# Kernel optimization log

Measured on AMD Instinct MI355X. Metric: run time of the kernel, lower is better.

The kernel has to match this reference:

```python
import jax, jax.numpy as jnp
import numpy as np

N_NODES = 50000
N_EDGES = 800000
IN_F = 128
HID = 16
HEADS = 8
OUT_F = 128


def setup_inputs() -> dict:
    key = jax.random.key(0)
    ks = jax.random.split(key, 16)
    h = jax.random.normal(ks[0], (N_NODES, IN_F), dtype=jnp.float32)
    src1 = jax.random.randint(ks[1], (N_EDGES,), 0, N_NODES, dtype=jnp.int32)
    dst1 = jax.random.randint(ks[2], (N_EDGES,), 0, N_NODES, dtype=jnp.int32)
    src2 = jax.random.randint(ks[3], (N_EDGES,), 0, N_NODES, dtype=jnp.int32)
    dst2 = jax.random.randint(ks[4], (N_EDGES,), 0, N_NODES, dtype=jnp.int32)
    norm1 = jax.random.uniform(ks[5], (N_NODES, 1), dtype=jnp.float32)
    norm2 = jax.random.uniform(ks[6], (N_NODES, 1), dtype=jnp.float32)
    D = HEADS * HID  # 128
    W_lin = jax.random.normal(ks[7], (IN_F, D), dtype=jnp.float32) * (1.0 / np.sqrt(IN_F))
    b_lin = jax.random.normal(ks[8], (D,), dtype=jnp.float32) * 0.01
    al = jax.random.normal(ks[9], (HEADS, HID, 1), dtype=jnp.float32) * 0.1
    ar = jax.random.normal(ks[10], (HEADS, HID, 1), dtype=jnp.float32) * 0.1
    W_fc = jax.random.normal(ks[11], (D, OUT_F), dtype=jnp.float32) * (1.0 / np.sqrt(D))
    b_fc = jax.random.normal(ks[12], (OUT_F,), dtype=jnp.float32) * 0.01
    return {"h": h, "src1": src1, "dst1": dst1, "src2": src2, "dst2": dst2,
            "norm1": norm1, "norm2": norm2, "W_lin": W_lin, "b_lin": b_lin,
            "al": al, "ar": ar, "W_fc": W_fc, "b_fc": b_fc}


def _propagate(feat, norm, src, dst, n_nodes):
    # msg = h[src] * norm[src]; accum[v] = sum_{e: dst=v} msg_e; out = accum * norm
    msg = feat[src] * norm[src]                      # [E, D]
    agg = jax.ops.segment_sum(msg, dst, num_segments=n_nodes)
    return agg * norm                                # [N, D]


def _leaky_relu(x):
    return jnp.where(x > 0, x, 0.2 * x)


def reference(h, src1, dst1, src2, dst2, norm1, norm2, W_lin, b_lin, al, ar, W_fc, b_fc):
    N = h.shape[0]
    hf = h @ W_lin + b_lin                           # [N, 8*HID] (dropout p given but eval-mode -> identity)
    h1 = _propagate(hf, norm1, src1, dst1, N)
    h2 = _propagate(hf, norm2, src2, dst2, N)
    # Faithful to torch: row-major reshape [N, 8*HID] -> (8, N, HID)
    h1r = h1.reshape(HEADS, N, HID)
    h2r = h2.reshape(HEADS, N, HID)
    hr = hf.reshape(HEADS, N, HID)
    ai = jnp.einsum('hnd,hdo->hno', hr, al)          # [8, N, 1]
    aj1 = jnp.einsum('hnd,hdo->hno', h1r, ar)
    aj2 = jnp.einsum('hnd,hdo->hno', h2r, ar)
    a1 = jnp.clip(jnp.exp(_leaky_relu(ai + aj1)), -10.0, 10.0)
    a2 = jnp.clip(jnp.exp(_leaky_relu(ai + aj2)), -10.0, 10.0)
    denom = a1 + a2
    out = (a1 / denom) * h1r + (a2 / denom) * h2r    # [8, N, HID]
    out = out.reshape(N, HEADS * HID)
    return out @ W_fc + b_fc
```

## Files before the change

### kernel.cpp

```cpp
#include <hip/hip_runtime.h>

#define NN 50000
#define NE 800000
#define NB 196
#define NBLK 512
#define CHUNK 1563
#define MAXB 6144

typedef __bf16 bf16x8 __attribute__((ext_vector_type(8)));
typedef float  f32x4  __attribute__((ext_vector_type(4)));

__device__ __forceinline__ unsigned short f2bf(float x) {
    unsigned u = __float_as_uint(x);
    return (unsigned short)((u + 0x7FFFu + ((u >> 16) & 1u)) >> 16);
}
__device__ __forceinline__ float bflo(unsigned u) { return __uint_as_float(u << 16); }
__device__ __forceinline__ float bfhi(unsigned u) { return __uint_as_float(u & 0xFFFF0000u); }

__global__ __launch_bounds__(256) void mfma_gemm_kernel(
    const float* __restrict__ X, const float* __restrict__ W,
    const float* __restrict__ bias, float* __restrict__ Y,
    unsigned short* __restrict__ Ybf, int nrows)
{
    __shared__ unsigned short Wt[128 * 136];
    __shared__ unsigned short Xh[64 * 136];
    __shared__ unsigned short Xl[64 * 136];
    const int t = threadIdx.x;
    const int lane = t & 63;
    const int wv = t >> 6;
    const int row0 = blockIdx.x * 64;
    const int m16 = lane & 15;
    const int quad = lane >> 4;

    for (int i = t; i < 128 * 128; i += 256) {
        int k = i >> 7, n = i & 127;
        Wt[n * 136 + k] = f2bf(W[i]);
    }
    {
        const float4* X4 = (const float4*)X;
        #pragma unroll
        for (int i = 0; i < 8; i++) {
            int idx = t + i * 256;
            int rr = idx >> 5, kk = (idx & 31) * 4;
            int row = row0 + rr;
            float4 v = make_float4(0.f, 0.f, 0.f, 0.f);
            if (row < nrows) v = X4[(long)row * 32 + (idx & 31)];
            ushort4 h, l;
            h.x = f2bf(v.x); l.x = f2bf(v.x - bflo(h.x));
            h.y = f2bf(v.y); l.y = f2bf(v.y - bflo(h.y));
            h.z = f2bf(v.z); l.z = f2bf(v.z - bflo(h.z));
            h.w = f2bf(v.w); l.w = f2bf(v.w - bflo(h.w));
            *(ushort4*)&Xh[rr * 136 + kk] = h;
            *(ushort4*)&Xl[rr * 136 + kk] = l;
        }
    }
    __syncthreads();

    f32x4 acc[8];
    #pragma unroll
    for (int nt = 0; nt < 8; nt++) acc[nt] = (f32x4){0.f, 0.f, 0.f, 0.f};

    const int arow = wv * 16 + m16;
    #pragma unroll
    for (int kc = 0; kc < 4; kc++) {
        const int ko = kc * 32 + quad * 8;
        bf16x8 ah = *(const bf16x8*)&Xh[arow * 136 + ko];
        bf16x8 al = *(const bf16x8*)&Xl[arow * 136 + ko];
        #pragma unroll
        for (int nt = 0; nt < 8; nt++) {
            bf16x8 b = *(const bf16x8*)&Wt[(nt * 16 + m16) * 136 + ko];
            acc[nt] = __builtin_amdgcn_mfma_f32_16x16x32_bf16(ah, b, acc[nt], 0, 0, 0);
            acc[nt] = __builtin_amdgcn_mfma_f32_16x16x32_bf16(al, b, acc[nt], 0, 0, 0);
        }
    }

    #pragma unroll
    for (int nt = 0; nt < 8; nt++) {
        const int col = nt * 16 + m16;
        const float bc = bias[col];
        #pragma unroll
        for (int r = 0; r < 4; r++) {
            int row = row0 + wv * 16 + quad * 4 + r;
            if (row < nrows) {
                float val = acc[nt][r] + bc;
                if (Y)   Y[(long)row * 128 + col] = val;
                if (Ybf) Ybf[(long)row * 128 + col] = f2bf(val);
            }
        }
    }
}

__global__ __launch_bounds__(256) void histA_kernel(
    const int* __restrict__ dst1, const int* __restrict__ dst2, int* __restrict__ histG)
{
    __shared__ int h[2 * NB];
    const int t = threadIdx.x, blk = blockIdx.x;
    for (int i = t; i < 2 * NB; i += 256) h[i] = 0;
    __syncthreads();
    const int base = blk * CHUNK;
    const int lim = min(CHUNK, NE - base);
    for (int i = t; i < lim; i += 256) {
        atomicAdd(&h[dst1[base + i] >> 8], 1);
        atomicAdd(&h[NB + (dst2[base + i] >> 8)], 1);
    }
    __syncthreads();
    for (int i = t; i < 2 * NB; i += 256)
        histG[(size_t)i * NBLK + blk] = h[i];
}

__global__ __launch_bounds__(512) void scanB1_kernel(int* __restrict__ histG, int* __restrict__ btot)
{
    __shared__ int s[NBLK];
    const int t = threadIdx.x, row = blockIdx.x;
    int v = histG[(size_t)row * NBLK + t];
    s[t] = v;
    __syncthreads();
    for (int off = 1; off < NBLK; off <<= 1) {
        int x = (t >= off) ? s[t - off] : 0;
        __syncthreads();
        s[t] += x;
        __syncthreads();
    }
    histG[(size_t)row * NBLK + t] = s[t] - v;
    if (t == NBLK - 1) btot[row] = s[t];
}

__global__ __launch_bounds__(256) void scanB2_kernel(const int* __restrict__ btot, int* __restrict__ bbase)
{
    __shared__ int sc[256];
    const int t = threadIdx.x;
    for (int g = 0; g < 2; g++) {
        int v = (t < NB) ? btot[g * NB + t] : 0;
        sc[t] = v;
        __syncthreads();
        for (int off = 1; off < 256; off <<= 1) {
            int x = (t >= off) ? sc[t - off] : 0;
            __syncthreads();
            sc[t] += x;
            __syncthreads();
        }
        if (t < NB) bbase[g * NB + t] = sc[t] - v;
        __syncthreads();
    }
}

__global__ __launch_bounds__(256) void scatterC_kernel(
    const int* __restrict__ src1, const int* __restrict__ dst1,
    const int* __restrict__ src2, const int* __restrict__ dst2,
    const int* __restrict__ histG, const int* __restrict__ bbase,
    unsigned int* __restrict__ bin1, unsigned int* __restrict__ bin2)
{
    __shared__ int pos[2 * NB];
    const int t = threadIdx.x, blk = blockIdx.x;
    for (int i = t; i < 2 * NB; i += 256)
        pos[i] = bbase[i] + histG[(size_t)i * NBLK + blk];
    __syncthreads();
    const int base = blk * CHUNK;
    const int lim = min(CHUNK, NE - base);
    for (int i = t; i < lim; i += 256) {
        int d = dst1[base + i], s = src1[base + i];
        int slot = atomicAdd(&pos[d >> 8], 1);
        bin1[slot] = ((unsigned)(d & 255) << 16) | (unsigned)s;
        d = dst2[base + i]; s = src2[base + i];
        slot = atomicAdd(&pos[NB + (d >> 8)], 1);
        bin2[slot] = ((unsigned)(d & 255) << 16) | (unsigned)s;
    }
}

__global__ __launch_bounds__(256) void bucket_sort_kernel(
    const unsigned int* __restrict__ bin1, const unsigned int* __restrict__ bin2,
    const int* __restrict__ bbase, const int* __restrict__ btot,
    unsigned short* __restrict__ csr1, int* __restrict__ start1, int* __restrict__ deg1,
    unsigned short* __restrict__ csr2, int* __restrict__ start2, int* __restrict__ deg2)
{
    __shared__ int lcnt[256];
    __shared__ int sc[256];
    __shared__ int oat[256];
    __shared__ unsigned short outb[MAXB];
    const int t = threadIdx.x;
    const int g = (blockIdx.x >= NB) ? 1 : 0;
    const int b = blockIdx.x - g * NB;
    const unsigned int* bin = g ? bin2 : bin1;
    unsigned short* csr = g ? csr2 : csr1;
    int* start = g ? start2 : start1;
    int* deg   = g ? deg2 : deg1;

    const int base = bbase[g * NB + b];
    const int tot = min(btot[g * NB + b], MAXB);

    lcnt[t] = 0;
    __syncthreads();
    for (int i = t; i < tot; i += 256) atomicAdd(&lcnt[bin[base + i] >> 16], 1);
    __syncthreads();
    sc[t] = lcnt[t];
    __syncthreads();
    for (int off = 1; off < 256; off <<= 1) {
        int x = (t >= off) ? sc[t - off] : 0;
        __syncthreads();
        sc[t] += x;
        __syncthreads();
    }
    const int ex = sc[t] - lcnt[t];
    oat[t] = ex;
    __syncthreads();
    for (int i = t; i < tot; i += 256) {
        unsigned v = bin[base + i];
        int slot = atomicAdd(&oat[v >> 16], 1);
        outb[slot] = (unsigned short)(v & 0xFFFFu);
    }
    __syncthreads();
    for (int i = t; i < tot; i += 256) csr[base + i] = outb[i];
    int nd = b * 256 + t;
    if (nd < NN) { start[nd] = base + ex; deg[nd] = lcnt[t]; }
}

__global__ __launch_bounds__(256) void gather_kernel(
    const unsigned int* __restrict__ hfb, const unsigned short* __restrict__ csr,
    const int* __restrict__ start, const int* __restrict__ deg,
    const float* __restrict__ norm, float* __restrict__ agg)
{
    int node = (blockIdx.x * 256 + threadIdx.x) >> 6;
    int lane = threadIdx.x & 63;
    if (node >= NN) return;
    int st = start[node];
    int dg = deg[node];
    float2 acc = make_float2(0.f, 0.f);
    int i = 0;
    for (; i + 4 <= dg; i += 4) {
        int s0 = csr[st + i], s1 = csr[st + i + 1], s2 = csr[st + i + 2], s3 = csr[st + i + 3];
        float n0 = norm[s0], n1 = norm[s1], n2 = norm[s2], n3 = norm[s3];
        unsigned u0 = hfb[(long)s0 * 64 + lane];
        unsigned u1 = hfb[(long)s1 * 64 + lane];
        unsigned u2 = hfb[(long)s2 * 64 + lane];
        unsigned u3 = hfb[(long)s3 * 64 + lane];
        acc.x = fmaf(bflo(u0), n0, acc.x); acc.y = fmaf(bfhi(u0), n0, acc.y);
        acc.x = fmaf(bflo(u1), n1, acc.x); acc.y = fmaf(bfhi(u1), n1, acc.y);
        acc.x = fmaf(bflo(u2), n2, acc.x); acc.y = fmaf(bfhi(u2), n2, acc.y);
        acc.x = fmaf(bflo(u3), n3, acc.x); acc.y = fmaf(bfhi(u3), n3, acc.y);
    }
    for (; i < dg; i++) {
        int s = csr[st + i];
        float nv = norm[s];
        unsigned u = hfb[(long)s * 64 + lane];
        acc.x = fmaf(bflo(u), nv, acc.x); acc.y = fmaf(bfhi(u), nv, acc.y);
    }
    ((float2*)agg)[(long)node * 64 + lane] = acc;
}

__global__ __launch_bounds__(256) void attention_kernel(
    const unsigned int* __restrict__ hfb, float* __restrict__ agg1,
    const float* __restrict__ agg2, const float* __restrict__ norm1,
    const float* __restrict__ norm2, const float* __restrict__ al,
    const float* __restrict__ ar)
{
    int gid = blockIdx.x * 256 + threadIdx.x;
    int m = gid >> 2;
    int j = gid & 3;
    if (m >= 8 * NN) return;
    int n = m >> 3;
    int head = m / NN;
    float n1 = norm1[n], n2v = norm2[n];
    uint2 u = ((const uint2*)hfb)[gid];
    float4 f = make_float4(bflo(u.x), bfhi(u.x), bflo(u.y), bfhi(u.y));
    float4 g1 = ((const float4*)agg1)[gid];
    float4 g2 = ((const float4*)agg2)[gid];
    g1.x *= n1; g1.y *= n1; g1.z *= n1; g1.w *= n1;
    g2.x *= n2v; g2.y *= n2v; g2.z *= n2v; g2.w *= n2v;
    float4 av = ((const float4*)al)[head * 4 + j];
    float4 rv = ((const float4*)ar)[head * 4 + j];
    float s_ai = f.x * av.x + f.y * av.y + f.z * av.z + f.w * av.w;
    float s1 = g1.x * rv.x + g1.y * rv.y + g1.z * rv.z + g1.w * rv.w;
    float s2 = g2.x * rv.x + g2.y * rv.y + g2.z * rv.z + g2.w * rv.w;
    s_ai += __shfl_xor(s_ai, 1); s_ai += __shfl_xor(s_ai, 2);
    s1   += __shfl_xor(s1, 1);   s1   += __shfl_xor(s1, 2);
    s2   += __shfl_xor(s2, 1);   s2   += __shfl_xor(s2, 2);
    float x1 = s_ai + s1; x1 = x1 > 0.f ? x1 : 0.2f * x1;
    float x2 = s_ai + s2; x2 = x2 > 0.f ? x2 : 0.2f * x2;
    float e1 = fminf(expf(x1), 10.f);
    float e2 = fminf(expf(x2), 10.f);
    float inv = 1.f / (e1 + e2);
    float w1 = e1 * inv, w2 = e2 * inv;
    float4 o;
    o.x = w1 * g1.x + w2 * g2.x;
    o.y = w1 * g1.y + w2 * g2.y;
    o.z = w1 * g1.z + w2 * g2.z;
    o.w = w1 * g1.w + w2 * g2.w;
    ((float4*)agg1)[gid] = o;
}

extern "C" void kernel_launch(void* const* d_in, const int* in_sizes, int n_in,
                              void* d_out, int out_size, void* d_ws, size_t ws_size,
                              hipStream_t stream)
{
    const float* h     = (const float*)d_in[0];
    const int*   src1  = (const int*)  d_in[1];
    const int*   dst1  = (const int*)  d_in[2];
    const int*   src2  = (const int*)  d_in[3];
    const int*   dst2  = (const int*)  d_in[4];
    const float* norm1 = (const float*)d_in[5];
    const float* norm2 = (const float*)d_in[6];
    const float* W_lin = (const float*)d_in[7];
    const float* b_lin = (const float*)d_in[8];
    const float* al    = (const float*)d_in[9];
    const float* ar    = (const float*)d_in[10];
    const float* W_fc  = (const float*)d_in[11];
    const float* b_fc  = (const float*)d_in[12];
    float* out = (float*)d_out;

    float* agg1 = (float*)d_ws;
    float* agg2 = agg1 + (size_t)NN * 128;
    unsigned int* bin1 = (unsigned int*)agg2;
    unsigned int* bin2 = bin1 + NE;
    unsigned short* hfb  = (unsigned short*)(agg2 + (size_t)NN * 128);
    unsigned short* csr1 = hfb + (size_t)NN * 128;
    unsigned short* csr2 = csr1 + NE;
    int* histG  = (int*)(csr2 + NE);
    int* btot   = histG + 2 * NB * NBLK;
    int* bbase  = btot + 2 * NB;
    int* start1 = bbase + 2 * NB;
    int* start2 = start1 + NN;
    int* deg1   = start2 + NN;
    int* deg2   = deg1 + NN;

    mfma_gemm_kernel<<<(NN + 63) / 64, 256, 0, stream>>>(h, W_lin, b_lin, nullptr, hfb, NN);

    histA_kernel<<<NBLK, 256, 0, stream>>>(dst1, dst2, histG);
    scanB1_kernel<<<2 * NB, NBLK, 0, stream>>>(histG, btot);
    scanB2_kernel<<<1, 256, 0, stream>>>(btot, bbase);
    scatterC_kernel<<<NBLK, 256, 0, stream>>>(src1, dst1, src2, dst2, histG, bbase, bin1, bin2);
    bucket_sort_kernel<<<2 * NB, 256, 0, stream>>>(bin1, bin2, bbase, btot,
                                                   csr1, start1, deg1,
                                                   csr2, start2, deg2);

    gather_kernel<<<(NN * 64 + 255) / 256, 256, 0, stream>>>((const unsigned int*)hfb, csr1, start1, deg1, norm1, agg1);
    gather_kernel<<<(NN * 64 + 255) / 256, 256, 0, stream>>>((const unsigned int*)hfb, csr2, start2, deg2, norm2, agg2);

    attention_kernel<<<8 * NN * 4 / 256, 256, 0, stream>>>((const unsigned int*)hfb, agg1, agg2,
                                                           norm1, norm2, al, ar);

    mfma_gemm_kernel<<<(NN + 63) / 64, 256, 0, stream>>>(agg1, W_fc, b_fc, out, nullptr, NN);
}
```

Before: 278.5 us.

## Pre-convert GEMM weights once, load A from registers, merge two gather launches

Adds a small kernel that transposes and converts both weight matrices to bf16 once, so each GEMM block no longer redoes the fp32-to-bf16 weight transpose. Weights are copied into a swizzled LDS tile, and the A operand is loaded straight into registers and split into hi/lo bf16 there, which drops the Xh/Xl LDS staging. The high half is now plain truncation rather than rounding, so the hi/lo split is slightly different. The two gather launches are merged into one kernel over both graphs to cut launch overhead and tail effects.

New measurement: 262.1 us. -5.9%, faster.

```diff
diff --git a/kernel.cpp b/kernel.cpp
--- a/kernel.cpp
+++ b/kernel.cpp
@@ -17,14 +17,31 @@
 __device__ __forceinline__ float bflo(unsigned u) { return __uint_as_float(u << 16); }
 __device__ __forceinline__ float bfhi(unsigned u) { return __uint_as_float(u & 0xFFFF0000u); }
 
+__global__ __launch_bounds__(256) void convert_w_kernel(
+    const float* __restrict__ Wa, const float* __restrict__ Wb,
+    unsigned short* __restrict__ Wta, unsigned short* __restrict__ Wtb)
+{
+    __shared__ float ls[128 * 132];
+    const float* W = blockIdx.x ? Wb : Wa;
+    unsigned short* Wt = blockIdx.x ? Wtb : Wta;
+    const int t = threadIdx.x;
+    for (int i = t; i < 128 * 32; i += 256) {
+        int k = i >> 5, n4 = i & 31;
+        *(float4*)&ls[k * 132 + n4 * 4] = ((const float4*)W)[i];
+    }
+    __syncthreads();
+    for (int j = t; j < 128 * 128; j += 256) {
+        int n = j >> 7, k = j & 127;
+        Wt[j] = f2bf(ls[k * 132 + n]);
+    }
+}
+
 __global__ __launch_bounds__(256) void mfma_gemm_kernel(
-    const float* __restrict__ X, const float* __restrict__ W,
+    const float* __restrict__ X, const unsigned short* __restrict__ Wt,
     const float* __restrict__ bias, float* __restrict__ Y,
     unsigned short* __restrict__ Ybf, int nrows)
 {
-    __shared__ unsigned short Wt[128 * 136];
-    __shared__ unsigned short Xh[64 * 136];
-    __shared__ unsigned short Xl[64 * 136];
+    __shared__ unsigned short Wl[128 * 128];
     const int t = threadIdx.x;
     const int lane = t & 63;
     const int wv = t >> 6;
@@ -32,26 +49,29 @@
     const int m16 = lane & 15;
     const int quad = lane >> 4;
 
-    for (int i = t; i < 128 * 128; i += 256) {
-        int k = i >> 7, n = i & 127;
-        Wt[n * 136 + k] = f2bf(W[i]);
-    }
     {
-        const float4* X4 = (const float4*)X;
+        const uint4* Wg = (const uint4*)Wt;
         #pragma unroll
         for (int i = 0; i < 8; i++) {
-            int idx = t + i * 256;
-            int rr = idx >> 5, kk = (idx & 31) * 4;
-            int row = row0 + rr;
-            float4 v = make_float4(0.f, 0.f, 0.f, 0.f);
-            if (row < nrows) v = X4[(long)row * 32 + (idx & 31)];
-            ushort4 h, l;
-            h.x = f2bf(v.x); l.x = f2bf(v.x - bflo(h.x));
-            h.y = f2bf(v.y); l.y = f2bf(v.y - bflo(h.y));
-            h.z = f2bf(v.z); l.z = f2bf(v.z - bflo(h.z));
-            h.w = f2bf(v.w); l.w = f2bf(v.w - bflo(h.w));
-            *(ushort4*)&Xh[rr * 136 + kk] = h;
-            *(ushort4*)&Xl[rr * 136 + kk] = l;
+            int gi = t + i * 256;
+            int n = gi >> 4, g = gi & 15;
+            uint4 v = Wg[gi];
+            *(uint4*)&Wl[n * 128 + (((g ^ (n & 15)) << 3))] = v;
+        }
+    }
+
+    const int arow = row0 + wv * 16 + m16;
+    const bool valid = (arow < nrows);
+    const float4* X4 = (const float4*)X;
+    float4 xr[8];
+    #pragma unroll
+    for (int kc = 0; kc < 4; kc++) {
+        if (valid) {
+            int gidx = arow * 32 + kc * 8 + quad * 2;
+            xr[kc * 2]     = X4[gidx];
+            xr[kc * 2 + 1] = X4[gidx + 1];
+        } else {
+            xr[kc * 2] = xr[kc * 2 + 1] = make_float4(0.f, 0.f, 0.f, 0.f);
         }
     }
     __syncthreads();
@@ -60,17 +80,24 @@
     #pragma unroll
     for (int nt = 0; nt < 8; nt++) acc[nt] = (f32x4){0.f, 0.f, 0.f, 0.f};
 
-    const int arow = wv * 16 + m16;
     #pragma unroll
     for (int kc = 0; kc < 4; kc++) {
-        const int ko = kc * 32 + quad * 8;
-        bf16x8 ah = *(const bf16x8*)&Xh[arow * 136 + ko];
-        bf16x8 al = *(const bf16x8*)&Xl[arow * 136 + ko];
+        union { unsigned short u[8]; bf16x8 v; } ah, al;
+        float f[8] = { xr[kc*2].x, xr[kc*2].y, xr[kc*2].z, xr[kc*2].w,
+                       xr[kc*2+1].x, xr[kc*2+1].y, xr[kc*2+1].z, xr[kc*2+1].w };
+        #pragma unroll
+        for (int j = 0; j < 8; j++) {
+            unsigned u = __float_as_uint(f[j]);
+            ah.u[j] = (unsigned short)(u >> 16);
+            al.u[j] = f2bf(f[j] - __uint_as_float(u & 0xFFFF0000u));
+        }
+        const int sgbase = (kc * 4 + quad);
         #pragma unroll
         for (int nt = 0; nt < 8; nt++) {
-            bf16x8 b = *(const bf16x8*)&Wt[(nt * 16 + m16) * 136 + ko];
-            acc[nt] = __builtin_amdgcn_mfma_f32_16x16x32_bf16(ah, b, acc[nt], 0, 0, 0);
-            acc[nt] = __builtin_amdgcn_mfma_f32_16x16x32_bf16(al, b, acc[nt], 0, 0, 0);
+            const int n = nt * 16 + m16;
+            bf16x8 b = *(const bf16x8*)&Wl[n * 128 + ((sgbase ^ m16) << 3)];
+            acc[nt] = __builtin_amdgcn_mfma_f32_16x16x32_bf16(ah.v, b, acc[nt], 0, 0, 0);
+            acc[nt] = __builtin_amdgcn_mfma_f32_16x16x32_bf16(al.v, b, acc[nt], 0, 0, 0);
         }
     }
 
@@ -214,14 +241,24 @@
     if (nd < NN) { start[nd] = base + ex; deg[nd] = lcnt[t]; }
 }
 
-__global__ __launch_bounds__(256) void gather_kernel(
-    const unsigned int* __restrict__ hfb, const unsigned short* __restrict__ csr,
-    const int* __restrict__ start, const int* __restrict__ deg,
-    const float* __restrict__ norm, float* __restrict__ agg)
-{
-    int node = (blockIdx.x * 256 + threadIdx.x) >> 6;
+__global__ __launch_bounds__(256) void gather_both_kernel(
+    const unsigned int* __restrict__ hfb,
+    const unsigned short* __restrict__ csr1, const int* __restrict__ start1,
+    const int* __restrict__ deg1, const float* __restrict__ norm1, float* __restrict__ agg1,
+    const unsigned short* __restrict__ csr2, const int* __restrict__ start2,
+    const int* __restrict__ deg2, const float* __restrict__ norm2, float* __restrict__ agg2)
+{
+    int w = (blockIdx.x * 256 + threadIdx.x) >> 6;
     int lane = threadIdx.x & 63;
-    if (node >= NN) return;
+    if (w >= 2 * NN) return;
+    const int g = (w >= NN);
+    const int node = w - g * NN;
+    const unsigned short* csr = g ? csr2 : csr1;
+    const int* start = g ? start2 : start1;
+    const int* deg   = g ? deg2 : deg1;
+    const float* norm = g ? norm2 : norm1;
+    float* agg = g ? agg2 : agg1;
+
     int st = start[node];
     int dg = deg[node];
     float2 acc = make_float2(0.f, 0.f);
@@ -314,7 +351,9 @@
     unsigned short* hfb  = (unsigned short*)(agg2 + (size_t)NN * 128);
     unsigned short* csr1 = hfb + (size_t)NN * 128;
     unsigned short* csr2 = csr1 + NE;
-    int* histG  = (int*)(csr2 + NE);
+    unsigned short* WtL  = csr2 + NE;
+    unsigned short* WtF  = WtL + 128 * 128;
+    int* histG  = (int*)(WtF + 128 * 128);
     int* btot   = histG + 2 * NB * NBLK;
     int* bbase  = btot + 2 * NB;
     int* start1 = bbase + 2 * NB;
@@ -322,7 +361,9 @@
     int* deg1   = start2 + NN;
     int* deg2   = deg1 + NN;
 
-    mfma_gemm_kernel<<<(NN + 63) / 64, 256, 0, stream>>>(h, W_lin, b_lin, nullptr, hfb, NN);
+    convert_w_kernel<<<2, 256, 0, stream>>>(W_lin, W_fc, WtL, WtF);
+
+    mfma_gemm_kernel<<<(NN + 63) / 64, 256, 0, stream>>>(h, WtL, b_lin, nullptr, hfb, NN);
 
     histA_kernel<<<NBLK, 256, 0, stream>>>(dst1, dst2, histG);
     scanB1_kernel<<<2 * NB, NBLK, 0, stream>>>(histG, btot);
@@ -332,11 +373,13 @@
                                                    csr1, start1, deg1,
                                                    csr2, start2, deg2);
 
-    gather_kernel<<<(NN * 64 + 255) / 256, 256, 0, stream>>>((const unsigned int*)hfb, csr1, start1, deg1, norm1, agg1);
-    gather_kernel<<<(NN * 64 + 255) / 256, 256, 0, stream>>>((const unsigned int*)hfb, csr2, start2, deg2, norm2, agg2);
+    gather_both_kernel<<<(2 * NN * 64 + 255) / 256, 256, 0, stream>>>(
+        (const unsigned int*)hfb,
+        csr1, start1, deg1, norm1, agg1,
+        csr2, start2, deg2, norm2, agg2);
 
     attention_kernel<<<8 * NN * 4 / 256, 256, 0, stream>>>((const unsigned int*)hfb, agg1, agg2,
                                                            norm1, norm2, al, ar);
 
-    mfma_gemm_kernel<<<(NN + 63) / 64, 256, 0, stream>>>(agg1, W_fc, b_fc, out, nullptr, NN);
-}
+    mfma_gemm_kernel<<<(NN + 63) / 64, 256, 0, stream>>>(agg1, WtF, b_fc, out, nullptr, NN);
+}
```
